# Performance work log

Measured on AMD Instinct MI355X. Metric: run time of the kernel, lower is better.

## Reference

```python
import jax, jax.numpy as jnp
import numpy as np

D_MODEL = 1024
N_HEAD = 16
D_K = D_MODEL // N_HEAD
D_FF = 2048
EPS = 1e-6
SCALE = np.sqrt(D_K).astype(np.float32)


def layer_norm(x, alpha, beta):
    # Faithful to source: unbiased std (ddof=1), eps added to std
    mean = jnp.mean(x, axis=-1, keepdims=True)
    std = jnp.std(x, axis=-1, keepdims=True, ddof=1) + EPS
    return alpha * (x - mean) / std + beta


def setup_inputs() -> dict:
    key = jax.random.key(0)
    ks = jax.random.split(key, 12)
    s = 0.02
    return {
        "x": jax.random.normal(ks[0], (4, 1024, D_MODEL), dtype=jnp.float32),
        "Wq": jax.random.normal(ks[1], (D_MODEL, D_MODEL), dtype=jnp.float32) * s,
        "bq": jax.random.normal(ks[2], (D_MODEL,), dtype=jnp.float32) * s,
        "Wo": jax.random.normal(ks[3], (D_MODEL, D_MODEL), dtype=jnp.float32) * s,
        "bo": jax.random.normal(ks[4], (D_MODEL,), dtype=jnp.float32) * s,
        "W1": jax.random.normal(ks[5], (D_MODEL, D_FF), dtype=jnp.float32) * s,
        "b1": jax.random.normal(ks[6], (D_FF,), dtype=jnp.float32) * s,
        "W2": jax.random.normal(ks[7], (D_FF, D_MODEL), dtype=jnp.float32) * s,
        "b2": jax.random.normal(ks[8], (D_MODEL,), dtype=jnp.float32) * s,
        "alpha": jnp.ones((D_MODEL,), dtype=jnp.float32),
        "beta": jnp.ones((D_MODEL,), dtype=jnp.float32),
    }


def reference(x, Wq, bq, Wo, bo, W1, b1, W2, b2, alpha, beta):
    b, s, d = x.shape
    # Source bug kept: q, k, v all use q_linear
    def proj(t):
        return (t @ Wq + bq).reshape(b, s, N_HEAD, D_K).transpose(0, 2, 1, 3)
    q = proj(x)  # [b,h,s,dk]
    k = proj(x)
    v = proj(x)
    scores = jnp.einsum('bhqd,bhkd->bhqk', q, k) / SCALE
    scores = jax.nn.softmax(scores, axis=-1)
    z = jnp.einsum('bhqk,bhkd->bhqd', scores, v)
    concat = z.transpose(0, 2, 1, 3).reshape(b, s, d)
    attn_out = concat @ Wo + bo
    x = layer_norm(x + attn_out, alpha, beta)
    ff = jax.nn.relu(x @ W1 + b1) @ W2 + b2
    x = layer_norm(x + ff, alpha, beta)  # source reuses norm_1
    return x
```

## Files before the change

kernel.cpp:

```cpp
#include <hip/hip_runtime.h>
#include <hip/hip_bf16.h>
#include <stdint.h>

#define TOK   4096
#define DMODEL 1024
#define DFF    2048
#define NHEAD  16
#define DK     64

typedef unsigned short u16;
typedef __attribute__((ext_vector_type(8))) short short8;
typedef __attribute__((ext_vector_type(4))) float f32x4;

typedef __attribute__((address_space(1))) void gvoid;
typedef __attribute__((address_space(3))) void lvoid;

#define QSCALE   0.35355339f
#define QUNSCALE 2.82842712f

__device__ __forceinline__ u16 f2b(float f) {
    uint32_t x = __builtin_bit_cast(uint32_t, f);
    x += 0x7FFFu + ((x >> 16) & 1u);
    return (u16)(x >> 16);
}
__device__ __forceinline__ float b2f(u16 u) {
    uint32_t x = ((uint32_t)u) << 16;
    return __builtin_bit_cast(float, x);
}
__device__ __forceinline__ uint32_t f2b2(float lo, float hi) {
    return (uint32_t)f2b(lo) | ((uint32_t)f2b(hi) << 16);
}

__device__ __forceinline__ void gload16(const void* g, void* l) {
    __builtin_amdgcn_global_load_lds((gvoid*)g, (lvoid*)l, 16, 0, 0);
}

template<int N>
__device__ __forceinline__ void wait_vm() {
    if constexpr (N == 0) asm volatile("s_waitcnt vmcnt(0)" ::: "memory");
    else if constexpr (N == 4) asm volatile("s_waitcnt vmcnt(4)" ::: "memory");
    else if constexpr (N == 6) asm volatile("s_waitcnt vmcnt(6)" ::: "memory");
}

__device__ __forceinline__ void cvt_tr_dev(
    const float* __restrict__ W, u16* __restrict__ Wt, int K, int N,
    int bx, int by, int tid, u16 (*T)[68])
{
    const int tx = tid & 15, ty = tid >> 4;
    const int n0 = bx * 64, k0 = by * 64;
#pragma unroll
    for (int i = 0; i < 4; i++) {
        int k = ty + i * 16;
        float4 v = *(const float4*)&W[(size_t)(k0 + k) * N + n0 + tx * 4];
        T[tx * 4 + 0][k] = f2b(v.x);
        T[tx * 4 + 1][k] = f2b(v.y);
        T[tx * 4 + 2][k] = f2b(v.z);
        T[tx * 4 + 3][k] = f2b(v.w);
    }
    __syncthreads();
#pragma unroll
    for (int i = 0; i < 4; i++) {
        int n = ty + i * 16;
        ushort4 o;
        o.x = T[n][tx * 4 + 0]; o.y = T[n][tx * 4 + 1];
        o.z = T[n][tx * 4 + 2]; o.w = T[n][tx * 4 + 3];
        *(ushort4*)&Wt[(size_t)(n0 + n) * K + k0 + tx * 4] = o;
    }
}

__global__ __launch_bounds__(256) void prep1(
    const float* __restrict__ Wq, u16* __restrict__ Wqt,
    const float* __restrict__ x, u16* __restrict__ xb)
{
    __shared__ u16 T[64][68];
    const int id = blockIdx.x, tid = threadIdx.x;
    if (id < 256) {
        cvt_tr_dev(Wq, Wqt, 1024, 1024, id & 15, id >> 4, tid, T);
    } else {
        size_t base = (size_t)(id - 256) * 1024 + tid;
#pragma unroll
        for (int j = 0; j < 4; j++) {
            float4 v = ((const float4*)x)[base + j * 256];
            ((uint2*)xb)[base + j * 256] =
                make_uint2(f2b2(v.x, v.y), f2b2(v.z, v.w));
        }
    }
}

template<int BM, int BN, bool RELU, bool OUTBF16, bool QOUT>
__global__ __launch_bounds__(256) void gemm_mfma(
    const u16* __restrict__ A, const u16* __restrict__ Bt,
    const float* __restrict__ bias, void* __restrict__ Cv,
    u16* __restrict__ CT, float oscale,
    int M, int N, int K)
{
    constexpr int MF = BM / 32;
    constexpr int NF = BN / 32;
    constexpr int LD = MF + NF;
    constexpr int ASTR = BM * 64;
    constexpr int BSTR = BN * 64;
    __shared__ __align__(16) u16 As[2 * ASTR];
    __shared__ __align__(16) u16 Bs[2 * BSTR];

    const int tid  = threadIdx.x;
    const int lane = tid & 63;
    const int wid  = tid >> 6;
    const int wm = wid >> 1, wn = wid & 1;
    const int frow = lane & 15, fk = lane >> 4;

    const int gx = N / BN;
    const int gy = M / BM;
    const int rpx = gy >> 3;
    const int L = blockIdx.x;
    const int xcd = L & 7, within = L >> 3;
    const int yy = xcd * rpx + within / gx;
    const int xx = within % gx;

    const int row0 = yy * BM;
    const int col0 = xx * BN;

    const u16* gA[MF]; u16* lA[MF];
    const u16* gB[NF]; u16* lB[NF];
#pragma unroll
    for (int inst = 0; inst < MF; inst++) {
        int s = inst * 256 + tid;
        int r = s >> 3;
        int kc = ((s & 7) ^ (r & 7)) * 8;
        gA[inst] = A + (size_t)(row0 + r) * K + kc;
        lA[inst] = As + inst * 2048 + wid * 512;
    }
#pragma unroll
    for (int inst = 0; inst < NF; inst++) {
        int s = inst * 256 + tid;
        int r = s >> 3;
        int kc = ((s & 7) ^ (r & 7)) * 8;
        gB[inst] = Bt + (size_t)(col0 + r) * K + kc;
        lB[inst] = Bs + inst * 2048 + wid * 512;
    }

    int aoff[MF][2], boff[NF][2];
#pragma unroll
    for (int m = 0; m < MF; m++) {
        int r = wm * (BM / 2) + m * 16 + frow;
#pragma unroll
        for (int kk = 0; kk < 2; kk++)
            aoff[m][kk] = r * 64 + (((kk << 2) + fk) ^ (r & 7)) * 8;
    }
#pragma unroll
    for (int n = 0; n < NF; n++) {
        int r = wn * (BN / 2) + n * 16 + frow;
#pragma unroll
        for (int kk = 0; kk < 2; kk++)
            boff[n][kk] = r * 64 + (((kk << 2) + fk) ^ (r & 7)) * 8;
    }

    f32x4 acc[MF][NF] = {};
    const int nT = K >> 6;

#pragma unroll
    for (int inst = 0; inst < MF; inst++) gload16(gA[inst], lA[inst]);
#pragma unroll
    for (int inst = 0; inst < NF; inst++) gload16(gB[inst], lB[inst]);
#pragma unroll
    for (int inst = 0; inst < MF; inst++) gload16(gA[inst] + 64, lA[inst] + ASTR);
#pragma unroll
    for (int inst = 0; inst < NF; inst++) gload16(gB[inst] + 64, lB[inst] + BSTR);
    wait_vm<LD>();
    __builtin_amdgcn_sched_barrier(0);
    __builtin_amdgcn_s_barrier();
    __builtin_amdgcn_sched_barrier(0);

    for (int t = 0; t < nT; t++) {
        const int cur = t & 1;
        const u16* Ab = As + cur * ASTR;
        const u16* Bb = Bs + cur * BSTR;
        short8 a[MF][2], b[NF][2];
#pragma unroll
        for (int m = 0; m < MF; m++)
#pragma unroll
            for (int kk = 0; kk < 2; kk++)
                a[m][kk] = *(const short8*)(Ab + aoff[m][kk]);
#pragma unroll
        for (int n = 0; n < NF; n++)
#pragma unroll
            for (int kk = 0; kk < 2; kk++)
                b[n][kk] = *(const short8*)(Bb + boff[n][kk]);

#pragma unroll
        for (int m = 0; m < MF; m++)
#pragma unroll
            for (int n = 0; n < NF; n++)
#pragma unroll
                for (int kk = 0; kk < 2; kk++)
                    acc[m][n] = __builtin_amdgcn_mfma_f32_16x16x32_bf16(
                        a[m][kk], b[n][kk], acc[m][n], 0, 0, 0);

        __builtin_amdgcn_sched_barrier(0);
        __builtin_amdgcn_s_barrier();
        __builtin_amdgcn_sched_barrier(0);

        if (t + 2 < nT) {
            const int k0 = (t + 2) << 6;
#pragma unroll
            for (int inst = 0; inst < MF; inst++)
                gload16(gA[inst] + k0, lA[inst] + cur * ASTR);
#pragma unroll
            for (int inst = 0; inst < NF; inst++)
                gload16(gB[inst] + k0, lB[inst] + cur * BSTR);
        }
        if (t + 1 < nT) {
            if (t + 2 < nT) wait_vm<LD>();
            else            wait_vm<0>();
            __builtin_amdgcn_sched_barrier(0);
            __builtin_amdgcn_s_barrier();
            __builtin_amdgcn_sched_barrier(0);
        }
    }

#pragma unroll
    for (int n = 0; n < NF; n++) {
        const int gcol = col0 + wn * (BN / 2) + n * 16 + frow;
        const float bv = bias[gcol];
#pragma unroll
        for (int m = 0; m < MF; m++) {
            const int grow0 = row0 + wm * (BM / 2) + m * 16 + fk * 4;
            float v[4];
#pragma unroll
            for (int i = 0; i < 4; i++) {
                v[i] = (acc[m][n][i] + bv) * oscale;
                if (RELU) v[i] = fmaxf(v[i], 0.0f);
                if (OUTBF16)
                    ((u16*)Cv)[(size_t)(grow0 + i) * N + gcol] = f2b(v[i]);
                else
                    ((float*)Cv)[(size_t)(grow0 + i) * N + gcol] = v[i];
            }
            if (QOUT) {
                const int hh = gcol >> 6, d = gcol & 63;
                const int bb = grow0 >> 10, sl = grow0 & 1023;
                *(uint2*)&CT[(((size_t)(bb * 16 + hh) * 64 + d) << 10) + sl] =
                    make_uint2(f2b2(v[0], v[1]), f2b2(v[2], v[3]));
            }
        }
    }
}

__global__ __launch_bounds__(256, 2) void attn_prepw(
    const u16* __restrict__ qb, const u16* __restrict__ qT,
    u16* __restrict__ zb,
    const float* __restrict__ Wo, const float* __restrict__ W1,
    const float* __restrict__ W2,
    u16* __restrict__ Wot, u16* __restrict__ W1t, u16* __restrict__ W2t)
{
    __shared__ __align__(16) u16 Ks[2][64 * 64];
    __shared__ __align__(16) u16 Kt[2][64 * 64];
    __shared__ __align__(16) u16 Ps[128 * 64];

    const int tid = threadIdx.x;
    const int id  = blockIdx.x;

    if (id >= 512) {
        u16 (*T)[68] = reinterpret_cast<u16 (*)[68]>(&Ks[0][0]);
        int t = id - 512;
        if (t < 256)       cvt_tr_dev(Wo, Wot, 1024, 1024, t & 15, t >> 4, tid, T);
        else if (t < 768)  { t -= 256; cvt_tr_dev(W1, W1t, 1024, 2048, t & 31, t >> 5, tid, T); }
        else               { t -= 768; cvt_tr_dev(W2, W2t, 2048, 1024, t & 15, t >> 4, tid, T); }
        return;
    }

    const int lane = tid & 63;
    const int w    = tid >> 6;
    const int frow = lane & 15, fk = lane >> 4;

    const int h  = id & 15;
    const int qt = (id >> 4) & 7;
    const int b  = id >> 7;
    const int q0 = qt * 128;

    const u16* qhead = qb + ((size_t)b * 1024) * 1024 + h * 64;
    const u16* thead = qT + ((size_t)(b * 16 + h) * 64) * 1024;

#pragma unroll
    for (int inst = 0; inst < 2; inst++) {
        int s = inst * 256 + tid, r = s >> 3, kc = ((s & 7) ^ (r & 7)) * 8;
        gload16(qhead + (size_t)r * 1024 + kc, Ks[0] + inst * 2048 + w * 512);
        gload16(thead + (size_t)r * 1024 + kc, Kt[0] + inst * 2048 + w * 512);
    }

    short8 qf[2][2];
#pragma unroll
    for (int m = 0; m < 2; m++) {
        int r = q0 + w * 32 + m * 16 + frow;
#pragma unroll
        for (int kk = 0; kk < 2; kk++)
            qf[m][kk] = *(const short8*)(qhead + (size_t)r * 1024 + kk * 32 + fk * 8);
    }

    float lp[2] = {};
    f32x4 o[2][4] = {};

    __syncthreads();

    for (int t = 0; t < 16; t++) {
        const int cur = t & 1;
        if (t < 15) {
            const int kv = (t + 1) * 64;
#pragma unroll
            for (int inst = 0; inst < 2; inst++) {
                int s = inst * 256 + tid, r = s >> 3, kc = ((s & 7) ^ (r & 7)) * 8;
                gload16(qhead + (size_t)(kv + r) * 1024 + kc,
                        Ks[cur ^ 1] + inst * 2048 + w * 512);
                gload16(thead + (size_t)r * 1024 + kv + kc,
                        Kt[cur ^ 1] + inst * 2048 + w * 512);
            }
        }

        short8 kf[4][2];
#pragma unroll
        for (int n = 0; n < 4; n++) {
            int r = n * 16 + frow;
#pragma unroll
            for (int kk = 0; kk < 2; kk++)
                kf[n][kk] = *(const short8*)(Ks[cur] + r * 64 +
                                             (((kk << 2) + fk) ^ (r & 7)) * 8);
        }
        f32x4 st[4][2] = {};
#pragma unroll
        for (int nk = 0; nk < 4; nk++)
#pragma unroll
            for (int mq = 0; mq < 2; mq++)
#pragma unroll
                for (int kk = 0; kk < 2; kk++)
                    st[nk][mq] = __builtin_amdgcn_mfma_f32_16x16x32_bf16(
                        kf[nk][kk], qf[mq][kk], st[nk][mq], 0, 0, 0);

#pragma unroll
        for (int mq = 0; mq < 2; mq++) {
            const int r = w * 32 + mq * 16 + frow;
            const int rb = r * 64, sw = (r & 7) << 3;
#pragma unroll
            for (int nk = 0; nk < 4; nk++) {
                float p0 = __expf(st[nk][mq][0]);
                float p1 = __expf(st[nk][mq][1]);
                float p2 = __expf(st[nk][mq][2]);
                float p3 = __expf(st[nk][mq][3]);
                lp[mq] += (p0 + p1) + (p2 + p3);
                *(uint2*)&Ps[rb + ((nk * 16 + fk * 4) ^ sw)] =
                    make_uint2(f2b2(p0, p1), f2b2(p2, p3));
            }
        }

        short8 pa[2][2], vf[4][2];
#pragma unroll
        for (int m = 0; m < 2; m++) {
            int r = w * 32 + m * 16 + frow;
#pragma unroll
            for (int kk = 0; kk < 2; kk++)
                pa[m][kk] = *(const short8*)(Ps + r * 64 +
                                             (((kk << 2) + fk) ^ (r & 7)) * 8);
        }
#pragma unroll
        for (int n = 0; n < 4; n++) {
            int r = n * 16 + frow;
#pragma unroll
            for (int kk = 0; kk < 2; kk++)
                vf[n][kk] = *(const short8*)(Kt[cur] + r * 64 +
                                             (((kk << 2) + fk) ^ (r & 7)) * 8);
        }
#pragma unroll
        for (int m = 0; m < 2; m++)
#pragma unroll
            for (int n = 0; n < 4; n++)
#pragma unroll
                for (int kk = 0; kk < 2; kk++)
                    o[m][n] = __builtin_amdgcn_mfma_f32_16x16x32_bf16(
                        pa[m][kk], vf[n][kk], o[m][n], 0, 0, 0);

        __syncthreads();
    }

#pragma unroll
    for (int mq = 0; mq < 2; mq++) {
        lp[mq] += __shfl_xor(lp[mq], 16);
        lp[mq] += __shfl_xor(lp[mq], 32);
    }
#pragma unroll
    for (int m = 0; m < 2; m++)
#pragma unroll
        for (int i = 0; i < 4; i++) {
            const float lfull = __shfl(lp[m], fk * 4 + i);
            const float rl = QUNSCALE / lfull;
            const size_t gr = (size_t)(b * 1024 + q0 + w * 32 + m * 16 + fk * 4 + i);
#pragma unroll
            for (int n = 0; n < 4; n++)
                zb[gr * 1024 + h * 64 + n * 16 + frow] = f2b(o[m][n][i] * rl);
        }
}

__device__ __forceinline__ float4 ld4(const float* p) { return *(const float4*)p; }
__device__ __forceinline__ float4 ld4(const u16* p) {
    ushort4 u = *(const ushort4*)p;
    return make_float4(b2f(u.x), b2f(u.y), b2f(u.z), b2f(u.w));
}
__device__ __forceinline__ void st4(float* p, float4 v) { *(float4*)p = v; }
__device__ __forceinline__ void st4(u16* p, float4 v) {
    *(uint2*)p = make_uint2(f2b2(v.x, v.y), f2b2(v.z, v.w));
}

template<typename TA, typename TB, typename TO>
__global__ __launch_bounds__(256) void add_ln(
    const TA* __restrict__ a, const TB* __restrict__ b,
    const float* __restrict__ alpha, const float* __restrict__ beta,
    TO* __restrict__ out)
{
    const int row = blockIdx.x;
    const int c = threadIdx.x * 4;
    float4 va = ld4(a + (size_t)row * DMODEL + c);
    float4 vb = ld4(b + (size_t)row * DMODEL + c);
    float v0 = va.x + vb.x, v1 = va.y + vb.y;
    float v2 = va.z + vb.z, v3 = va.w + vb.w;

    float sum = (v0 + v1) + (v2 + v3);
    float sq  = (v0 * v0 + v1 * v1) + (v2 * v2 + v3 * v3);
#pragma unroll
    for (int off = 32; off > 0; off >>= 1) {
        sum += __shfl_xor(sum, off);
        sq  += __shfl_xor(sq, off);
    }
    __shared__ float s1[4], s2[4];
    const int wid = threadIdx.x >> 6, lane = threadIdx.x & 63;
    if (lane == 0) { s1[wid] = sum; s2[wid] = sq; }
    __syncthreads();
    sum = (s1[0] + s1[1]) + (s1[2] + s1[3]);
    sq  = (s2[0] + s2[1]) + (s2[2] + s2[3]);

    const float mean = sum * (1.0f / 1024.0f);
    float var = (sq - 1024.0f * mean * mean) * (1.0f / 1023.0f);
    var = fmaxf(var, 0.0f);
    const float rdenom = 1.0f / (sqrtf(var) + 1e-6f);

    float4 al = *(const float4*)(alpha + c);
    float4 be = *(const float4*)(beta + c);
    float4 r;
    r.x = al.x * (v0 - mean) * rdenom + be.x;
    r.y = al.y * (v1 - mean) * rdenom + be.y;
    r.z = al.z * (v2 - mean) * rdenom + be.z;
    r.w = al.w * (v3 - mean) * rdenom + be.w;
    st4(out + (size_t)row * DMODEL + c, r);
}

extern "C" void kernel_launch(void* const* d_in, const int* in_sizes, int n_in,
                              void* d_out, int out_size, void* d_ws, size_t ws_size,
                              hipStream_t stream) {
    const float* x     = (const float*)d_in[0];
    const float* Wq    = (const float*)d_in[1];
    const float* bq    = (const float*)d_in[2];
    const float* Wo    = (const float*)d_in[3];
    const float* bo    = (const float*)d_in[4];
    const float* W1    = (const float*)d_in[5];
    const float* b1    = (const float*)d_in[6];
    const float* W2    = (const float*)d_in[7];
    const float* b2    = (const float*)d_in[8];
    const float* alpha = (const float*)d_in[9];
    const float* beta  = (const float*)d_in[10];

    char* base = (char*)d_ws;
    u16* Wqt = (u16*)base;
    u16* Wot = (u16*)(base + (2u  << 20));
    u16* W1t = (u16*)(base + (4u  << 20));
    u16* W2t = (u16*)(base + (8u  << 20));
    u16* zb  = (u16*)(base + (12u << 20));
    u16* x1b = zb;
    u16* qb  = (u16*)(base + (20u << 20));
    u16* g2  = qb;
    u16* qT  = (u16*)(base + (28u << 20));
    u16* xb  = (u16*)(base + (36u << 20));
    u16* g   = xb;
    u16* hb  = (u16*)(base + (36u << 20));

    dim3 blk(256);

    prep1<<<dim3(1280), blk, 0, stream>>>(Wq, Wqt, x, xb);

    gemm_mfma<64, 64, false, true, true><<<dim3(1024), blk, 0, stream>>>(
        xb, Wqt, bq, qb, qT, QSCALE, TOK, 1024, 1024);
    attn_prepw<<<dim3(1792), blk, 0, stream>>>(
        qb, qT, zb, Wo, W1, W2, Wot, W1t, W2t);
    gemm_mfma<64, 64, false, true, false><<<dim3(1024), blk, 0, stream>>>(
        zb, Wot, bo, g, nullptr, 1.0f, TOK, 1024, 1024);
    add_ln<float, u16, u16><<<dim3(TOK), blk, 0, stream>>>(x, g, alpha, beta, x1b);
    gemm_mfma<64, 128, true, true, false><<<dim3(1024), blk, 0, stream>>>(
        x1b, W1t, b1, hb, nullptr, 1.0f, TOK, 2048, 1024);
    gemm_mfma<64, 64, false, true, false><<<dim3(1024), blk, 0, stream>>>(
        hb, W2t, b2, g2, nullptr, 1.0f, TOK, 1024, 2048);
    add_ln<u16, u16, float><<<dim3(TOK), blk, 0, stream>>>(
        x1b, g2, alpha, beta, (float*)d_out);
}
```

Baseline: 143.4 us.

## Enlarge GEMM tiles, simplify prefetch pipeline, raise MFMA priority, read bf16 residual

Switches all GEMMs to 128-row tiles with half as many blocks, which raises data reuse per block. The GEMM main loop changes from a two-ahead prefetch with explicit vmcnt waits to a simpler one-ahead prefetch guarded by __syncthreads, which may expose more load latency. The attention kernel wraps its MFMA sections in s_setprio to favour matrix issue. The first add+layernorm now reads the bf16 copy of x instead of fp32, which cuts traffic at some precision cost, and its input buffer is moved to avoid aliasing.

```diff
diff --git a/kernel.cpp b/kernel.cpp
--- a/kernel.cpp
+++ b/kernel.cpp
@@ -33,13 +33,6 @@
 
 __device__ __forceinline__ void gload16(const void* g, void* l) {
     __builtin_amdgcn_global_load_lds((gvoid*)g, (lvoid*)l, 16, 0, 0);
-}
-
-template<int N>
-__device__ __forceinline__ void wait_vm() {
-    if constexpr (N == 0) asm volatile("s_waitcnt vmcnt(0)" ::: "memory");
-    else if constexpr (N == 4) asm volatile("s_waitcnt vmcnt(4)" ::: "memory");
-    else if constexpr (N == 6) asm volatile("s_waitcnt vmcnt(6)" ::: "memory");
 }
 
 __device__ __forceinline__ void cvt_tr_dev(
@@ -96,7 +89,6 @@
 {
     constexpr int MF = BM / 32;
     constexpr int NF = BN / 32;
-    constexpr int LD = MF + NF;
     constexpr int ASTR = BM * 64;
     constexpr int BSTR = BN * 64;
     __shared__ __align__(16) u16 As[2 * ASTR];
@@ -161,17 +153,20 @@
     for (int inst = 0; inst < MF; inst++) gload16(gA[inst], lA[inst]);
 #pragma unroll
     for (int inst = 0; inst < NF; inst++) gload16(gB[inst], lB[inst]);
-#pragma unroll
-    for (int inst = 0; inst < MF; inst++) gload16(gA[inst] + 64, lA[inst] + ASTR);
-#pragma unroll
-    for (int inst = 0; inst < NF; inst++) gload16(gB[inst] + 64, lB[inst] + BSTR);
-    wait_vm<LD>();
-    __builtin_amdgcn_sched_barrier(0);
-    __builtin_amdgcn_s_barrier();
-    __builtin_amdgcn_sched_barrier(0);
+    __syncthreads();
 
     for (int t = 0; t < nT; t++) {
         const int cur = t & 1;
+        if (t + 1 < nT) {
+            const int k0 = (t + 1) << 6;
+#pragma unroll
+            for (int inst = 0; inst < MF; inst++)
+                gload16(gA[inst] + k0, lA[inst] + (cur ^ 1) * ASTR);
+#pragma unroll
+            for (int inst = 0; inst < NF; inst++)
+                gload16(gB[inst] + k0, lB[inst] + (cur ^ 1) * BSTR);
+        }
+
         const u16* Ab = As + cur * ASTR;
         const u16* Bb = Bs + cur * BSTR;
         short8 a[MF][2], b[NF][2];
@@ -195,26 +190,7 @@
                     acc[m][n] = __builtin_amdgcn_mfma_f32_16x16x32_bf16(
                         a[m][kk], b[n][kk], acc[m][n], 0, 0, 0);
 
-        __builtin_amdgcn_sched_barrier(0);
-        __builtin_amdgcn_s_barrier();
-        __builtin_amdgcn_sched_barrier(0);
-
-        if (t + 2 < nT) {
-            const int k0 = (t + 2) << 6;
-#pragma unroll
-            for (int inst = 0; inst < MF; inst++)
-                gload16(gA[inst] + k0, lA[inst] + cur * ASTR);
-#pragma unroll
-            for (int inst = 0; inst < NF; inst++)
-                gload16(gB[inst] + k0, lB[inst] + cur * BSTR);
-        }
-        if (t + 1 < nT) {
-            if (t + 2 < nT) wait_vm<LD>();
-            else            wait_vm<0>();
-            __builtin_amdgcn_sched_barrier(0);
-            __builtin_amdgcn_s_barrier();
-            __builtin_amdgcn_sched_barrier(0);
-        }
+        __syncthreads();
     }
 
 #pragma unroll
@@ -324,6 +300,7 @@
                                              (((kk << 2) + fk) ^ (r & 7)) * 8);
         }
         f32x4 st[4][2] = {};
+        __builtin_amdgcn_s_setprio(1);
 #pragma unroll
         for (int nk = 0; nk < 4; nk++)
 #pragma unroll
@@ -332,6 +309,7 @@
                 for (int kk = 0; kk < 2; kk++)
                     st[nk][mq] = __builtin_amdgcn_mfma_f32_16x16x32_bf16(
                         kf[nk][kk], qf[mq][kk], st[nk][mq], 0, 0, 0);
+        __builtin_amdgcn_s_setprio(0);
 
 #pragma unroll
         for (int mq = 0; mq < 2; mq++) {
@@ -366,6 +344,7 @@
                 vf[n][kk] = *(const short8*)(Kt[cur] + r * 64 +
                                              (((kk << 2) + fk) ^ (r & 7)) * 8);
         }
+        __builtin_amdgcn_s_setprio(1);
 #pragma unroll
         for (int m = 0; m < 2; m++)
 #pragma unroll
@@ -374,6 +353,7 @@
                 for (int kk = 0; kk < 2; kk++)
                     o[m][n] = __builtin_amdgcn_mfma_f32_16x16x32_bf16(
                         pa[m][kk], vf[n][kk], o[m][n], 0, 0, 0);
+        __builtin_amdgcn_s_setprio(0);
 
         __syncthreads();
     }
@@ -473,24 +453,24 @@
     u16* qb  = (u16*)(base + (20u << 20));
     u16* g2  = qb;
     u16* qT  = (u16*)(base + (28u << 20));
+    u16* g   = qT;
     u16* xb  = (u16*)(base + (36u << 20));
-    u16* g   = xb;
     u16* hb  = (u16*)(base + (36u << 20));
 
     dim3 blk(256);
 
     prep1<<<dim3(1280), blk, 0, stream>>>(Wq, Wqt, x, xb);
 
-    gemm_mfma<64, 64, false, true, true><<<dim3(1024), blk, 0, stream>>>(
+    gemm_mfma<128, 64, false, true, true><<<dim3(512), blk, 0, stream>>>(
         xb, Wqt, bq, qb, qT, QSCALE, TOK, 1024, 1024);
     attn_prepw<<<dim3(1792), blk, 0, stream>>>(
         qb, qT, zb, Wo, W1, W2, Wot, W1t, W2t);
-    gemm_mfma<64, 64, false, true, false><<<dim3(1024), blk, 0, stream>>>(
+    gemm_mfma<128, 64, false, true, false><<<dim3(512), blk, 0, stream>>>(
         zb, Wot, bo, g, nullptr, 1.0f, TOK, 1024, 1024);
-    add_ln<float, u16, u16><<<dim3(TOK), blk, 0, stream>>>(x, g, alpha, beta, x1b);
-    gemm_mfma<64, 128, true, true, false><<<dim3(1024), blk, 0, stream>>>(
+    add_ln<u16, u16, u16><<<dim3(TOK), blk, 0, stream>>>(xb, g, alpha, beta, x1b);
+    gemm_mfma<128, 128, true, true, false><<<dim3(512), blk, 0, stream>>>(
         x1b, W1t, b1, hb, nullptr, 1.0f, TOK, 2048, 1024);
-    gemm_mfma<64, 64, false, true, false><<<dim3(1024), blk, 0, stream>>>(
+    gemm_mfma<128, 64, false, true, false><<<dim3(512), blk, 0, stream>>>(
         hb, W2t, b2, g2, nullptr, 1.0f, TOK, 1024, 2048);
     add_ln<u16, u16, float><<<dim3(TOK), blk, 0, stream>>>(
         x1b, g2, alpha, beta, (float*)d_out);
```

New measurement: 143.8 us. About the same (+0.3%).
